# Kernel tuning notes

Measured on AMD Instinct MI355X. Metric: run time of the kernel, lower is better.

The kernel has to match this reference:

```python
import jax, jax.numpy as jnp
import numpy as np

B, N, M, H, D, DIM = 4, 2048, 512, 12, 64, 768
INNER = H * D
SCALE = D ** -0.5
NEG = -1e9
TEMP = 24.0


def setup_inputs() -> dict:
    key = jax.random.key(0)
    ks = jax.random.split(key, 8)
    x = jax.random.normal(ks[0], (B, N, DIM), jnp.float32)
    kx = jax.random.normal(ks[1], (B, M, DIM), jnp.float32)
    krd = jax.random.uniform(ks[2], (B, H, M, N), jnp.float32)
    clst = jax.random.normal(ks[3], (B, 1, DIM), jnp.float32)
    att_mask = jax.random.randint(ks[4], (B, H, N, M), 0, 2) > 0
    W_qkv = jax.random.normal(ks[5], (DIM, 3 * INNER), jnp.float32) / np.sqrt(DIM)
    W_out = jax.random.normal(ks[6], (INNER, DIM), jnp.float32) / np.sqrt(INNER)
    b_out = jnp.zeros((DIM,), jnp.float32)
    return {"x": x, "kx": kx, "krd": krd, "clst": clst, "att_mask": att_mask,
            "W_qkv": W_qkv, "W_out": W_out, "b_out": b_out}


def _qkv(t, W_qkv):
    # [b, n, dim] -> three [b, h, n, d]
    b, n, _ = t.shape
    qkv = (t @ W_qkv).reshape(b, n, 3, H, D)
    qkv = jnp.moveaxis(qkv, 2, 0)            # [3, b, n, h, d]
    qkv = jnp.transpose(qkv, (0, 1, 3, 2, 4))  # [3, b, h, n, d]
    return qkv[0], qkv[1], qkv[2]


def _merge(t):
    # [b, h, n, d] -> [b, n, h*d]
    b, h, n, d = t.shape
    return jnp.transpose(t, (0, 2, 1, 3)).reshape(b, n, h * d)


def reference(x, kx, krd, clst, att_mask, W_qkv, W_out, b_out):
    t_q, t_k, t_v = _qkv(x, W_qkv)
    k_q, k_k, k_v = _qkv(kx, W_qkv)
    c_q, _, _ = _qkv(clst, W_qkv)

    krd_T = jnp.transpose(krd, (0, 1, 3, 2))  # [b, h, N, M]

    # branch 1: instance queries vs kernel keys
    dots = jnp.einsum('bhid,bhjd->bhij', t_q, k_k) * SCALE
    dots = jnp.where(att_mask, NEG, dots)
    attn_hot = jax.nn.softmax(dots * TEMP, axis=-1) * krd_T
    attn = jax.nn.softmax(dots, axis=-1) * krd_T
    att_out = _merge(jnp.einsum('bhij,bhjd->bhid', attn, k_v))

    # branch 2: kernel queries vs instance keys
    k_dots = jnp.einsum('bhid,bhjd->bhij', k_q, t_k) * SCALE
    k_dots = jnp.where(jnp.transpose(att_mask, (0, 1, 3, 2)), NEG, k_dots)
    k_attn = jax.nn.softmax(k_dots, axis=-1) * krd
    k_out = _merge(jnp.einsum('bhij,bhjd->bhid', k_attn, t_v))

    # branch 3: cluster query vs kernel keys
    c_dots = jnp.einsum('bhid,bhjd->bhij', c_q, k_k) * SCALE
    c_dots = jnp.where(att_mask[:, :, :1], NEG, c_dots)
    c_attn = jax.nn.softmax(c_dots, axis=-1)
    c_out = _merge(jnp.einsum('bhij,bhjd->bhid', c_attn, k_v))

    proj = lambda t: t @ W_out + b_out
    return (proj(att_out), proj(k_out), proj(c_out),
            jnp.transpose(attn_hot, (0, 1, 3, 2)))
```

## Files before the change

kernel.cpp:

```cpp
#include <hip/hip_runtime.h>
#include <hip/hip_bf16.h>
#include <cmath>
#include <cstdint>

#define B_ 4
#define N_ 2048
#define M_ 512
#define H_ 12
#define D_ 64
#define DIM_ 768
#define QKV_ 2304
#define SCALE_ 0.125f
#define NEG_ -1e9f
#define TEMP_ 24.0f

typedef __attribute__((ext_vector_type(8))) short bf16x8;
typedef __attribute__((ext_vector_type(4))) float f32x4;

__device__ __forceinline__ short f2bf(float f) {
  union { float f; unsigned u; } v; v.f = f;
  unsigned r = v.u + 0x7fffu + ((v.u >> 16) & 1u);
  return (short)(r >> 16);
}
__device__ __forceinline__ float bf2f(short s) {
  union { unsigned u; float f; } v; v.u = ((unsigned)(unsigned short)s) << 16;
  return v.f;
}
#define MFMA16(a, b, c) __builtin_amdgcn_mfma_f32_16x16x32_bf16(a, b, c, 0, 0, 0)

__device__ __forceinline__ int xcd_swizzle(int orig, int nwg) {
  int qd = nwg >> 3, r = nwg & 7;
  int xcd = orig & 7, pos = orig >> 3;
  return (xcd < r ? xcd * (qd + 1) : r * (qd + 1) + (xcd - r) * qd) + pos;
}

__global__ __launch_bounds__(256) void wsplit_t(
    const float* __restrict__ W, int K, int Ncols,
    short* __restrict__ Wt_h, short* __restrict__ Wt_l) {
  __shared__ float t[32][33];
  const int n0 = blockIdx.x * 32, k0 = blockIdx.y * 32;
  const int tid = threadIdx.x;
  for (int e = tid; e < 1024; e += 256) {
    int r = e >> 5, c = e & 31;
    t[r][c] = W[(size_t)(k0 + r) * Ncols + n0 + c];
  }
  __syncthreads();
  for (int e = tid; e < 1024; e += 256) {
    int r = e >> 5, c = e & 31;
    float f = t[c][r];
    short hi = f2bf(f);
    short lo = f2bf(f - bf2f(hi));
    size_t o = (size_t)(n0 + r) * K + k0 + c;
    Wt_h[o] = hi; Wt_l[o] = lo;
  }
}

__global__ __launch_bounds__(256) void fsplit(
    const float* __restrict__ in, short* __restrict__ ho,
    short* __restrict__ lo_, int n4) {
  int stride = gridDim.x * 256;
  for (int i = blockIdx.x * 256 + threadIdx.x; i < n4; i += stride) {
    float4 f = ((const float4*)in)[i];
    short h0 = f2bf(f.x), h1 = f2bf(f.y), h2 = f2bf(f.z), h3 = f2bf(f.w);
    short l0 = f2bf(f.x - bf2f(h0)), l1 = f2bf(f.y - bf2f(h1));
    short l2 = f2bf(f.z - bf2f(h2)), l3 = f2bf(f.w - bf2f(h3));
    ((short4*)ho)[i] = make_short4(h0, h1, h2, h3);
    ((short4*)lo_)[i] = make_short4(l0, l1, l2, l3);
  }
}

__global__ __launch_bounds__(256) void mask_pack(
    const int* __restrict__ mask, unsigned* __restrict__ pm) {
  const size_t total = (size_t)B_ * H_ * N_ * M_;
  const size_t stride = (size_t)gridDim.x * blockDim.x;
  const int lane = threadIdx.x & 63;
  for (size_t i = (size_t)blockIdx.x * blockDim.x + threadIdx.x; i < total;
       i += stride) {
    unsigned long long bal = __ballot(mask[i] != 0);
    if (lane == 0) *(unsigned long long*)(pm + (i >> 5)) = bal;
  }
}

__global__ __launch_bounds__(256) void qkv_mfma(
    const short* __restrict__ Ahp, const short* __restrict__ Alp,
    const short* __restrict__ Wth, const short* __restrict__ Wtl,
    int rowsPerB, int totalRows,
    short* __restrict__ qh, short* __restrict__ ql,
    short* __restrict__ kh, short* __restrict__ kl,
    short* __restrict__ vt) {
  __shared__ __align__(16) short As_h[128 * 40], As_l[128 * 40];
  __shared__ __align__(16) short Bs_h[128 * 40], Bs_l[128 * 40];
  const int nwg = gridDim.x * gridDim.y;
  const int nb = xcd_swizzle(blockIdx.y * gridDim.x + blockIdx.x, nwg);
  const int gx = gridDim.x;
  const int r0 = (nb / gx) * 128, c0 = (nb % gx) * 128;
  const int tid = threadIdx.x;
  const int w = tid >> 6, ln = tid & 63, q = ln >> 4, l15 = ln & 15;
  const int wM = (w & 1) * 64, wN = (w >> 1) * 64;
  const f32x4 z = {0.f, 0.f, 0.f, 0.f};
  f32x4 acc[4][4];
  for (int i = 0; i < 4; i++)
    for (int j = 0; j < 4; j++) acc[i][j] = z;
  for (int k0 = 0; k0 < DIM_; k0 += 32) {
    for (int e = tid; e < 512; e += 256) {
      int row = e >> 2, c = e & 3;
      int ar = r0 + row; if (ar >= totalRows) ar = totalRows - 1;
      size_t ga = (size_t)ar * DIM_ + k0 + c * 8;
      size_t gb = (size_t)(c0 + row) * DIM_ + k0 + c * 8;
      int o = row * 40 + c * 8;
      *(uint4*)(As_h + o) = *(const uint4*)(Ahp + ga);
      *(uint4*)(As_l + o) = *(const uint4*)(Alp + ga);
      *(uint4*)(Bs_h + o) = *(const uint4*)(Wth + gb);
      *(uint4*)(Bs_l + o) = *(const uint4*)(Wtl + gb);
    }
    __syncthreads();
    bf16x8 ah[4], al[4], bhf[4], blf[4];
    for (int mt = 0; mt < 4; mt++) {
      int o = (wM + mt * 16 + l15) * 40 + q * 8;
      ah[mt] = *(const bf16x8*)(As_h + o);
      al[mt] = *(const bf16x8*)(As_l + o);
    }
    for (int nt = 0; nt < 4; nt++) {
      int o = (wN + nt * 16 + l15) * 40 + q * 8;
      bhf[nt] = *(const bf16x8*)(Bs_h + o);
      blf[nt] = *(const bf16x8*)(Bs_l + o);
    }
    for (int mt = 0; mt < 4; mt++)
      for (int nt = 0; nt < 4; nt++) {
        f32x4 c = acc[mt][nt];
        c = MFMA16(ah[mt], bhf[nt], c);
        c = MFMA16(ah[mt], blf[nt], c);
        c = MFMA16(al[mt], bhf[nt], c);
        acc[mt][nt] = c;
      }
    __syncthreads();
  }
  for (int mt = 0; mt < 4; mt++)
    for (int nt = 0; nt < 4; nt++)
      for (int r = 0; r < 4; r++) {
        int gr = r0 + wM + mt * 16 + q * 4 + r;
        if (gr >= totalRows) continue;
        int gc = c0 + wN + nt * 16 + l15;
        int which = gc / DIM_;
        int rem = gc - which * DIM_;
        int hh = rem >> 6, d = rem & 63;
        int b = gr / rowsPerB, n = gr - b * rowsPerB;
        float v = acc[mt][nt][r];
        short hi = f2bf(v);
        if (which == 2) {
          vt[(((size_t)b * H_ + hh) * 64 + d) * rowsPerB + n] = hi;
        } else {
          short lo = f2bf(v - bf2f(hi));
          size_t o = (((size_t)b * H_ + hh) * rowsPerB + n) * 64 + d;
          if (which == 0) { qh[o] = hi; ql[o] = lo; }
          else           { kh[o] = hi; kl[o] = lo; }
        }
      }
}

__global__ __launch_bounds__(256) void proj_mfma(
    const short* __restrict__ Ahp, const short* __restrict__ Alp,
    const short* __restrict__ Bth, const short* __restrict__ Btl,
    const float* __restrict__ bias, float* __restrict__ C, int totalRows) {
  __shared__ __align__(16) short As_h[128 * 40], As_l[128 * 40];
  __shared__ __align__(16) short Bs_h[128 * 40], Bs_l[128 * 40];
  const int nwg = gridDim.x * gridDim.y;
  const int nb = xcd_swizzle(blockIdx.y * gridDim.x + blockIdx.x, nwg);
  const int gx = gridDim.x;
  const int r0 = (nb / gx) * 128, c0 = (nb % gx) * 128;
  const int tid = threadIdx.x;
  const int w = tid >> 6, ln = tid & 63, q = ln >> 4, l15 = ln & 15;
  const int wM = (w & 1) * 64, wN = (w >> 1) * 64;
  const f32x4 z = {0.f, 0.f, 0.f, 0.f};
  f32x4 acc[4][4];
  for (int i = 0; i < 4; i++)
    for (int j = 0; j < 4; j++) acc[i][j] = z;
  for (int k0 = 0; k0 < DIM_; k0 += 32) {
    for (int e = tid; e < 512; e += 256) {
      int row = e >> 2, c = e & 3;
      int ar = r0 + row; if (ar >= totalRows) ar = totalRows - 1;
      size_t ga = (size_t)ar * DIM_ + k0 + c * 8;
      size_t gb = (size_t)(c0 + row) * DIM_ + k0 + c * 8;
      int o = row * 40 + c * 8;
      *(uint4*)(As_h + o) = *(const uint4*)(Ahp + ga);
      *(uint4*)(As_l + o) = *(const uint4*)(Alp + ga);
      *(uint4*)(Bs_h + o) = *(const uint4*)(Bth + gb);
      *(uint4*)(Bs_l + o) = *(const uint4*)(Btl + gb);
    }
    __syncthreads();
    bf16x8 ah[4], al[4], bhf[4], blf[4];
    for (int mt = 0; mt < 4; mt++) {
      int o = (wM + mt * 16 + l15) * 40 + q * 8;
      ah[mt] = *(const bf16x8*)(As_h + o);
      al[mt] = *(const bf16x8*)(As_l + o);
    }
    for (int nt = 0; nt < 4; nt++) {
      int o = (wN + nt * 16 + l15) * 40 + q * 8;
      bhf[nt] = *(const bf16x8*)(Bs_h + o);
      blf[nt] = *(const bf16x8*)(Bs_l + o);
    }
    for (int mt = 0; mt < 4; mt++)
      for (int nt = 0; nt < 4; nt++) {
        f32x4 c = acc[mt][nt];
        c = MFMA16(ah[mt], bhf[nt], c);
        c = MFMA16(ah[mt], blf[nt], c);
        c = MFMA16(al[mt], bhf[nt], c);
        acc[mt][nt] = c;
      }
    __syncthreads();
  }
  for (int mt = 0; mt < 4; mt++)
    for (int nt = 0; nt < 4; nt++)
      for (int r = 0; r < 4; r++) {
        int gr = r0 + wM + mt * 16 + q * 4 + r;
        if (gr >= totalRows) continue;
        int gc = c0 + wN + nt * 16 + l15;
        C[(size_t)gr * DIM_ + gc] = acc[mt][nt][r] + bias[gc];
      }
}

__global__ __launch_bounds__(512, 4) void branch1_mfma(
    const short* __restrict__ tqh, const short* __restrict__ tql,
    const short* __restrict__ kkh, const short* __restrict__ kkl,
    const short* __restrict__ kvt, const float* __restrict__ krd,
    const unsigned* __restrict__ pm, float* __restrict__ out3,
    short* __restrict__ amh, short* __restrict__ aml) {
  __shared__ __align__(16) float sc[32 * 520];
  __shared__ unsigned mskw[512];
  __shared__ float rowM[32], inv1[32], inv2[32];
  short* P2h = (short*)sc;
  short* P2l = P2h + 32 * 520;
  const int b = blockIdx.z, h = blockIdx.y, n0 = blockIdx.x * 32;
  const size_t bhi = (size_t)b * H_ + h;
  const int tid = threadIdx.x;
  const int w = tid >> 6, ln = tid & 63, q = ln >> 4, l15 = ln & 15;
  const float* krd0 = krd + bhi * M_ * N_;
  mskw[tid] = pm[(bhi * N_ + n0) * 16 + tid];
  {
    bf16x8 ah[2][2], al[2][2];
    for (int mt = 0; mt < 2; mt++) {
      const short* ap = tqh + ((bhi * N_ + n0 + mt * 16 + l15) * D_ + q * 8);
      const short* ap2 = tql + ((bhi * N_ + n0 + mt * 16 + l15) * D_ + q * 8);
      ah[mt][0] = *(const bf16x8*)(ap);
      ah[mt][1] = *(const bf16x8*)(ap + 32);
      al[mt][0] = *(const bf16x8*)(ap2);
      al[mt][1] = *(const bf16x8*)(ap2 + 32);
    }
    for (int t = 0; t < 4; t++) {
      int ct = w * 4 + t;
      const short* bp = kkh + ((bhi * M_ + ct * 16 + l15) * D_ + q * 8);
      const short* bp2 = kkl + ((bhi * M_ + ct * 16 + l15) * D_ + q * 8);
      bf16x8 bh0 = *(const bf16x8*)(bp);
      bf16x8 bh1 = *(const bf16x8*)(bp + 32);
      bf16x8 bl0 = *(const bf16x8*)(bp2);
      bf16x8 bl1 = *(const bf16x8*)(bp2 + 32);
      for (int mt = 0; mt < 2; mt++) {
        f32x4 a = {0.f, 0.f, 0.f, 0.f};
        a = MFMA16(ah[mt][0], bh0, a); a = MFMA16(ah[mt][1], bh1, a);
        a = MFMA16(ah[mt][0], bl0, a); a = MFMA16(ah[mt][1], bl1, a);
        a = MFMA16(al[mt][0], bh0, a); a = MFMA16(al[mt][1], bh1, a);
        for (int r = 0; r < 4; r++) {
          int row = mt * 16 + q * 4 + r;
          sc[row * 520 + ((ct * 16 + l15) ^ ((row >> 2) & 7))] = a[r];
        }
      }
    }
  }
  const int pi = tid & 31, pg = tid >> 5;
  float kr[32];
#pragma unroll
  for (int t = 0; t < 32; t++)
    kr[t] = __builtin_nontemporal_load(
        krd0 + (size_t)(pg * 32 + t) * N_ + n0 + pi);
  __syncthreads();
  {
    int i = tid >> 4, jl = tid & 15;
    int sw = (i >> 2) & 7;
    float* scr = sc + i * 520;
    const unsigned* mrow = mskw + i * 16;
    float mx = -INFINITY;
    for (int j = jl; j < M_; j += 16) {
      float dv = scr[j ^ sw];
      dv = ((mrow[j >> 5] >> (j & 31)) & 1) ? NEG_ : dv * SCALE_;
      scr[j ^ sw] = dv;
      mx = fmaxf(mx, dv);
    }
    for (int o = 8; o >= 1; o >>= 1) mx = fmaxf(mx, __shfl_xor(mx, o, 16));
    float s1 = 0.f, s2 = 0.f;
    for (int j = jl; j < M_; j += 16) {
      float e2 = __expf(scr[j ^ sw] - mx);
      scr[j ^ sw] = e2;
      float x2 = e2 * e2, x4 = x2 * x2, x8 = x4 * x4, x16 = x8 * x8;
      s1 += x16 * x8;
      s2 += e2;
    }
    for (int o = 8; o >= 1; o >>= 1) {
      s1 += __shfl_xor(s1, o, 16);
      s2 += __shfl_xor(s2, o, 16);
    }
    if (jl == 0) { inv1[i] = 1.f / s1; inv2[i] = 1.f / s2; }
  }
  __syncthreads();
  {
    float rv[32];
    int sw2 = (pi >> 2) & 7;
#pragma unroll
    for (int t = 0; t < 32; t++)
      rv[t] = sc[pi * 520 + ((pg * 32 + t) ^ sw2)];
    __syncthreads();
    float v1 = inv1[pi], v2 = inv2[pi];
    float* o3 = out3 + bhi * M_ * N_ + n0 + pi;
#pragma unroll
    for (int t = 0; t < 32; t += 2) {
      int j = pg * 32 + t;
      float e2a = rv[t], e2b = rv[t + 1];
      float a2 = e2a * e2a, a4 = a2 * a2, a8 = a4 * a4, a16 = a8 * a8;
      float b2 = e2b * e2b, b4 = b2 * b2, b8 = b4 * b4, b16 = b8 * b8;
      __builtin_nontemporal_store(a16 * a8 * v1 * kr[t], o3 + (size_t)j * N_);
      __builtin_nontemporal_store(b16 * b8 * v1 * kr[t + 1],
                                  o3 + (size_t)(j + 1) * N_);
      float p0 = e2a * v2 * kr[t];
      float p1 = e2b * v2 * kr[t + 1];
      short h0 = f2bf(p0), h1 = f2bf(p1);
      short lo0 = f2bf(p0 - bf2f(h0)), lo1 = f2bf(p1 - bf2f(h1));
      *(short2*)(P2h + pi * 520 + j) = make_short2(h0, h1);
      *(short2*)(P2l + pi * 520 + j) = make_short2(lo0, lo1);
    }
  }
  __syncthreads();
  {
    const int dc = w & 3, nh = w >> 2;
    f32x4 o0 = {0.f, 0.f, 0.f, 0.f}, o1 = {0.f, 0.f, 0.f, 0.f};
    const short* vbase = kvt + ((bhi * 64 + dc * 16 + l15) * (size_t)M_ + q * 8);
    const short* ph = P2h + (nh * 16 + l15) * 520 + q * 8;
    const short* pl = P2l + (nh * 16 + l15) * 520 + q * 8;
    for (int kc = 0; kc < 16; kc += 2) {
      bf16x8 pa0 = *(const bf16x8*)(ph + kc * 32);
      bf16x8 pl0 = *(const bf16x8*)(pl + kc * 32);
      bf16x8 bv0 = *(const bf16x8*)(vbase + kc * 32);
      o0 = MFMA16(pa0, bv0, o0);
      o0 = MFMA16(pl0, bv0, o0);
      bf16x8 pa1 = *(const bf16x8*)(ph + (kc + 1) * 32);
      bf16x8 pl1 = *(const bf16x8*)(pl + (kc + 1) * 32);
      bf16x8 bv1 = *(const bf16x8*)(vbase + (kc + 1) * 32);
      o1 = MFMA16(pa1, bv1, o1);
      o1 = MFMA16(pl1, bv1, o1);
    }
    o0 += o1;
    for (int r = 0; r < 4; r++) {
      float v = o0[r];
      short hi = f2bf(v), lo = f2bf(v - bf2f(hi));
      size_t o = ((size_t)b * N_ + n0 + nh * 16 + q * 4 + r) * DIM_ +
                 h * 64 + dc * 16 + l15;
      amh[o] = hi; aml[o] = lo;
    }
  }
}

__global__ __launch_bounds__(256) void branch2_mfma(
    const short* __restrict__ kqh, const short* __restrict__ kql,
    const short* __restrict__ tkh, const short* __restrict__ tkl,
    const short* __restrict__ tvt, const float* __restrict__ krd,
    const unsigned* __restrict__ pm, short* __restrict__ kmh,
    short* __restrict__ kml) {
  __shared__ __align__(16) float sc[32 * 136];
  __shared__ unsigned mskw[128];
  __shared__ float rowM[32], rowL[32], alph[32];
  short* P2h = (short*)sc;
  short* P2l = P2h + 32 * 136;
  const int b = blockIdx.z, h = blockIdx.y, m0 = blockIdx.x * 32;
  const size_t bhi = (size_t)b * H_ + h;
  const int tid = threadIdx.x;
  const int w = tid >> 6, ln = tid & 63, q = ln >> 4, l15 = ln & 15;
  const float* krd0 = krd + (bhi * M_ + m0) * N_;
  const int mword = m0 >> 5;
  bf16x8 Ah[2][2], Al[2][2];
  for (int mt = 0; mt < 2; mt++)
    for (int kc = 0; kc < 2; kc++) {
      size_t o = (bhi * M_ + m0 + mt * 16 + l15) * D_ + kc * 32 + q * 8;
      Ah[mt][kc] = *(const bf16x8*)(kqh + o);
      Al[mt][kc] = *(const bf16x8*)(kql + o);
    }
  if (tid < 32) { rowM[tid] = -INFINITY; rowL[tid] = 0.f; }
  const f32x4 z = {0.f, 0.f, 0.f, 0.f};
  f32x4 oa[2]; oa[0] = z; oa[1] = z;
  __syncthreads();
  for (int n0 = 0; n0 < N_; n0 += 128) {
    if (tid < 128) mskw[tid] = pm[(bhi * N_ + n0 + tid) * 16 + mword];
    for (int t = 0; t < 2; t++) {
      int ct = w * 2 + t;
      const short* bp = tkh + ((bhi * N_ + n0 + ct * 16 + l15) * D_ + q * 8);
      const short* bp2 = tkl + ((bhi * N_ + n0 + ct * 16 + l15) * D_ + q * 8);
      bf16x8 bh0 = *(const bf16x8*)(bp), bh1 = *(const bf16x8*)(bp + 32);
      bf16x8 bl0 = *(const bf16x8*)(bp2), bl1 = *(const bf16x8*)(bp2 + 32);
      for (int mt = 0; mt < 2; mt++) {
        f32x4 a = {0.f, 0.f, 0.f, 0.f};
        a = MFMA16(Ah[mt][0], bh0, a); a = MFMA16(Ah[mt][1], bh1, a);
        a = MFMA16(Ah[mt][0], bl0, a); a = MFMA16(Ah[mt][1], bl1, a);
        a = MFMA16(Al[mt][0], bh0, a); a = MFMA16(Al[mt][1], bh1, a);
        for (int r = 0; r < 4; r++)
          sc[(mt * 16 + q * 4 + r) * 136 + ct * 16 + l15] = a[r];
      }
    }
    __syncthreads();
    {
      int i = tid >> 3, jl = tid & 7;
      float mx = -INFINITY;
      for (int j = jl; j < 128; j += 8) {
        float s = sc[i * 136 + j];
        s = ((mskw[j] >> i) & 1) ? NEG_ : s * SCALE_;
        sc[i * 136 + j] = s;
        mx = fmaxf(mx, s);
      }
      for (int o = 4; o >= 1; o >>= 1) mx = fmaxf(mx, __shfl_xor(mx, o, 8));
      float mold = rowM[i];
      float mnew = fmaxf(mold, mx);
      float sum = 0.f;
      for (int j = jl; j < 128; j += 8) {
        float p = __expf(sc[i * 136 + j] - mnew);
        sc[i * 136 + j] = p;
        sum += p;
      }
      for (int o = 4; o >= 1; o >>= 1) sum += __shfl_xor(sum, o, 8);
      if (jl == 0) {
        float al = (mold == -INFINITY) ? 0.f : __expf(mold - mnew);
        alph[i] = al;
        rowL[i] = rowL[i] * al + sum;
        rowM[i] = mnew;
      }
    }
    __syncthreads();
    {
      float rv[16], kv2[16];
      const int j = tid & 127;
      const int ib = tid >> 7;
#pragma unroll
      for (int t = 0; t < 16; t++) {
        rv[t] = sc[(ib + 2 * t) * 136 + j];
        kv2[t] = __builtin_nontemporal_load(
            krd0 + (size_t)(ib + 2 * t) * N_ + n0 + j);
      }
      __syncthreads();
#pragma unroll
      for (int t = 0; t < 16; t++) {
        int i = ib + 2 * t;
        float p2 = rv[t] * kv2[t];
        short hi = f2bf(p2), lo = f2bf(p2 - bf2f(hi));
        P2h[i * 136 + j] = hi;
        P2l[i * 136 + j] = lo;
      }
    }
    __syncthreads();
    {
      for (int mt = 0; mt < 2; mt++) {
        f32x4 t = oa[mt];
        for (int r = 0; r < 4; r++) t[r] *= alph[mt * 16 + q * 4 + r];
        for (int kc = 0; kc < 4; kc++) {
          bf16x8 pa = *(const bf16x8*)(P2h + (mt * 16 + l15) * 136 + kc * 32 + q * 8);
          bf16x8 pl = *(const bf16x8*)(P2l + (mt * 16 + l15) * 136 + kc * 32 + q * 8);
          bf16x8 bv = *(const bf16x8*)(tvt + ((bhi * 64 + w * 16 + l15) * (size_t)N_ + n0 + kc * 32 + q * 8));
          t = MFMA16(pa, bv, t);
          t = MFMA16(pl, bv, t);
        }
        oa[mt] = t;
      }
    }
    __syncthreads();
  }
  for (int mt = 0; mt < 2; mt++)
    for (int r = 0; r < 4; r++) {
      int row = mt * 16 + q * 4 + r;
      float v = oa[mt][r] / rowL[row];
      short hi = f2bf(v), lo = f2bf(v - bf2f(hi));
      size_t o = ((size_t)b * M_ + m0 + row) * DIM_ + h * 64 + w * 16 + l15;
      kmh[o] = hi; kml[o] = lo;
    }
}

__global__ __launch_bounds__(256) void branch3_k(
    const short* __restrict__ cqh, const short* __restrict__ cql,
    const short* __restrict__ kkh, const short* __restrict__ kkl,
    const short* __restrict__ kvt, const unsigned* __restrict__ pm,
    short* __restrict__ cmh, short* __restrict__ cml) {
  const int h = blockIdx.x, b = blockIdx.y;
  __shared__ float qv[64];
  __shared__ float p[512];
  __shared__ float wr1[4], wr2[4];
  __shared__ float ored[4][64];
  const size_t bhi = (size_t)b * H_ + h;
  const int tid = threadIdx.x;
  if (tid < 64) qv[tid] = bf2f(cqh[bhi * 64 + tid]) + bf2f(cql[bhi * 64 + tid]);
  __syncthreads();
  const unsigned* m0p = pm + bhi * N_ * 16;
  for (int j = tid; j < 512; j += 256) {
    float acc = 0;
    for (int kk = 0; kk < 64; kk++)
      acc += qv[kk] * (bf2f(kkh[(bhi * M_ + j) * 64 + kk]) +
                       bf2f(kkl[(bhi * M_ + j) * 64 + kk]));
    acc *= SCALE_;
    if ((m0p[j >> 5] >> (j & 31)) & 1) acc = NEG_;
    p[j] = acc;
  }
  __syncthreads();
  float mx = fmaxf(p[tid], p[tid + 256]);
  for (int o = 32; o >= 1; o >>= 1) mx = fmaxf(mx, __shfl_xor(mx, o, 64));
  if ((tid & 63) == 0) wr1[tid >> 6] = mx;
  __syncthreads();
  mx = fmaxf(fmaxf(wr1[0], wr1[1]), fmaxf(wr1[2], wr1[3]));
  float e0 = __expf(p[tid] - mx), e1 = __expf(p[tid + 256] - mx);
  float s = e0 + e1;
  for (int o = 32; o >= 1; o >>= 1) s += __shfl_xor(s, o, 64);
  p[tid] = e0; p[tid + 256] = e1;
  if ((tid & 63) == 0) wr2[tid >> 6] = s;
  __syncthreads();
  float invS = 1.f / (wr2[0] + wr2[1] + wr2[2] + wr2[3]);
  int dd = tid & 63, gg = tid >> 6;
  float o = 0;
  for (int j = gg; j < 512; j += 4)
    o += p[j] * bf2f(kvt[(bhi * 64 + dd) * (size_t)M_ + j]);
  ored[gg][dd] = o;
  __syncthreads();
  if (gg == 0) {
    float r = (ored[0][dd] + ored[1][dd] + ored[2][dd] + ored[3][dd]) * invS;
    short hi = f2bf(r), lo = f2bf(r - bf2f(hi));
    cmh[(size_t)b * DIM_ + h * 64 + dd] = hi;
    cml[(size_t)b * DIM_ + h * 64 + dd] = lo;
  }
}

extern "C" void kernel_launch(void* const* d_in, const int* in_sizes, int n_in,
                              void* d_out, int out_size, void* d_ws,
                              size_t ws_size, hipStream_t stream) {
  const float* x = (const float*)d_in[0];
  const float* kx = (const float*)d_in[1];
  const float* krd = (const float*)d_in[2];
  const float* clst = (const float*)d_in[3];
  const int* mask = (const int*)d_in[4];
  const float* Wqkv = (const float*)d_in[5];
  const float* Wout = (const float*)d_in[6];
  const float* bout = (const float*)d_in[7];

  short* p = (short*)d_ws;
  auto alloc = [&](size_t n) { short* r = p; p += n; return r; };
  short* Wq_h = alloc(2304ull * 768); short* Wq_l = alloc(2304ull * 768);
  short* Wo_h = alloc(768ull * 768);  short* Wo_l = alloc(768ull * 768);
  short* tq_h = alloc(6291456); short* tq_l = alloc(6291456);
  short* tk_h = alloc(6291456); short* tk_l = alloc(6291456);
  short* tv_t = alloc(6291456);
  short* kq_h = alloc(1572864); short* kq_l = alloc(1572864);
  short* kk_h = alloc(1572864); short* kk_l = alloc(1572864);
  short* kv_t = alloc(1572864);
  short* cq_h = alloc(3072); short* cq_l = alloc(3072);
  short* ck_h = alloc(3072); short* ck_l = alloc(3072);
  short* cv_t = alloc(3072);
  short* am_h = alloc(6291456); short* am_l = alloc(6291456);
  short* km_h = alloc(1572864); short* km_l = alloc(1572864);
  short* cm_h = alloc(3072); short* cm_l = alloc(3072);

  float* out0 = (float*)d_out;
  float* out1 = out0 + 6291456;
  float* out2 = out1 + 1572864;
  float* out3 = out2 + 3072;

  wsplit_t<<<dim3(72, 24), 256, 0, stream>>>(Wqkv, DIM_, QKV_, Wq_h, Wq_l);
  wsplit_t<<<dim3(24, 24), 256, 0, stream>>>(Wout, DIM_, DIM_, Wo_h, Wo_l);

  short* xs_h = am_h, *xs_l = am_l;
  short* kxs_h = km_h, *kxs_l = km_l;
  short* cs_h = cm_h, *cs_l = cm_l;
  fsplit<<<dim3(2048), 256, 0, stream>>>(x, xs_h, xs_l, B_ * N_ * DIM_ / 4);
  fsplit<<<dim3(1536), 256, 0, stream>>>(kx, kxs_h, kxs_l, B_ * M_ * DIM_ / 4);
  fsplit<<<dim3(3), 256, 0, stream>>>(clst, cs_h, cs_l, B_ * DIM_ / 4);

  qkv_mfma<<<dim3(18, 64), 256, 0, stream>>>(xs_h, xs_l, Wq_h, Wq_l, N_,
                                             B_ * N_, tq_h, tq_l, tk_h, tk_l,
                                             tv_t);
  qkv_mfma<<<dim3(18, 16), 256, 0, stream>>>(kxs_h, kxs_l, Wq_h, Wq_l, M_,
                                             B_ * M_, kq_h, kq_l, kk_h, kk_l,
                                             kv_t);
  qkv_mfma<<<dim3(18, 1), 256, 0, stream>>>(cs_h, cs_l, Wq_h, Wq_l, 1, B_,
                                            cq_h, cq_l, ck_h, ck_l, cv_t);

  unsigned* pmask = (unsigned*)Wq_h;
  mask_pack<<<dim3(2048), 256, 0, stream>>>(mask, pmask);

  branch1_mfma<<<dim3(N_ / 32, H_, B_), 512, 0, stream>>>(
      tq_h, tq_l, kk_h, kk_l, kv_t, krd, pmask, out3, am_h, am_l);
  branch2_mfma<<<dim3(M_ / 32, H_, B_), 256, 0, stream>>>(
      kq_h, kq_l, tk_h, tk_l, tv_t, krd, pmask, km_h, km_l);
  branch3_k<<<dim3(H_, B_), 256, 0, stream>>>(cq_h, cq_l, kk_h, kk_l, kv_t,
                                              pmask, cm_h, cm_l);

  proj_mfma<<<dim3(6, 64), 256, 0, stream>>>(am_h, am_l, Wo_h, Wo_l, bout,
                                             out0, B_ * N_);
  proj_mfma<<<dim3(6, 16), 256, 0, stream>>>(km_h, km_l, Wo_h, Wo_l, bout,
                                             out1, B_ * M_);
  proj_mfma<<<dim3(6, 1), 256, 0, stream>>>(cm_h, cm_l, Wo_h, Wo_l, bout,
                                            out2, B_);
}
```

Before: 1.207 ms.

## Split branch2 attention over key dimension with separate combine kernel

Branch 2 previously ran one block per 32 kernel-query rows per head (768 blocks), each looping over all 2048 instance keys. The loop is now split four ways along the key dimension, giving four times as many blocks, each writing partial outputs plus row max and sum to scratch. A new combine kernel merges the partials with log-sum-exp weighting and writes the hi/lo bf16 outputs. This raises occupancy and parallelism on a long serial loop, at the cost of an extra launch and scratch traffic; the scratch reuses the out0/out1 buffers before the projection kernels overwrite them.

After: 1.168 ms. 1.03x faster.

```diff
diff --git a/kernel.cpp b/kernel.cpp
--- a/kernel.cpp
+++ b/kernel.cpp
@@ -13,6 +13,7 @@
 #define SCALE_ 0.125f
 #define NEG_ -1e9f
 #define TEMP_ 24.0f
+#define NSPLIT_ 4
 
 typedef __attribute__((ext_vector_type(8))) short bf16x8;
 typedef __attribute__((ext_vector_type(4))) float f32x4;
@@ -361,15 +362,18 @@
     const short* __restrict__ kqh, const short* __restrict__ kql,
     const short* __restrict__ tkh, const short* __restrict__ tkl,
     const short* __restrict__ tvt, const float* __restrict__ krd,
-    const unsigned* __restrict__ pm, short* __restrict__ kmh,
-    short* __restrict__ kml) {
+    const unsigned* __restrict__ pm, float* __restrict__ pO,
+    float* __restrict__ pML) {
   __shared__ __align__(16) float sc[32 * 136];
   __shared__ unsigned mskw[128];
   __shared__ float rowM[32], rowL[32], alph[32];
   short* P2h = (short*)sc;
   short* P2l = P2h + 32 * 136;
-  const int b = blockIdx.z, h = blockIdx.y, m0 = blockIdx.x * 32;
+  const int b = blockIdx.z, h = blockIdx.y;
+  const int mblk = blockIdx.x >> 2, split = blockIdx.x & 3;
+  const int m0 = mblk * 32;
   const size_t bhi = (size_t)b * H_ + h;
+  const int pidx = ((int)bhi * 16 + mblk) * NSPLIT_ + split;
   const int tid = threadIdx.x;
   const int w = tid >> 6, ln = tid & 63, q = ln >> 4, l15 = ln & 15;
   const float* krd0 = krd + (bhi * M_ + m0) * N_;
@@ -385,7 +389,8 @@
   const f32x4 z = {0.f, 0.f, 0.f, 0.f};
   f32x4 oa[2]; oa[0] = z; oa[1] = z;
   __syncthreads();
-  for (int n0 = 0; n0 < N_; n0 += 128) {
+  const int nbeg = split * (N_ / NSPLIT_), nend = nbeg + N_ / NSPLIT_;
+  for (int n0 = nbeg; n0 < nend; n0 += 128) {
     if (tid < 128) mskw[tid] = pm[(bhi * N_ + n0 + tid) * 16 + mword];
     for (int t = 0; t < 2; t++) {
       int ct = w * 2 + t;
@@ -467,14 +472,64 @@
     }
     __syncthreads();
   }
+  float* po = pO + (size_t)pidx * 2048;
   for (int mt = 0; mt < 2; mt++)
     for (int r = 0; r < 4; r++) {
       int row = mt * 16 + q * 4 + r;
-      float v = oa[mt][r] / rowL[row];
-      short hi = f2bf(v), lo = f2bf(v - bf2f(hi));
-      size_t o = ((size_t)b * M_ + m0 + row) * DIM_ + h * 64 + w * 16 + l15;
-      kmh[o] = hi; kml[o] = lo;
-    }
+      po[row * 64 + w * 16 + l15] = oa[mt][r];
+    }
+  if (tid < 32) {
+    pML[(size_t)pidx * 64 + tid] = rowM[tid];
+    pML[(size_t)pidx * 64 + 32 + tid] = rowL[tid];
+  }
+}
+
+__global__ __launch_bounds__(256) void b2_combine(
+    const float* __restrict__ pO, const float* __restrict__ pML,
+    short* __restrict__ kmh, short* __restrict__ kml) {
+  const int mblk = blockIdx.x, h = blockIdx.y, b = blockIdx.z;
+  const size_t bhi = (size_t)b * H_ + h;
+  const int base = ((int)bhi * 16 + mblk) * NSPLIT_;
+  __shared__ float mS[NSPLIT_][32], lS[NSPLIT_][32], wgt[NSPLIT_][32], invL[32];
+  const int tid = threadIdx.x;
+  if (tid < 32 * NSPLIT_) {
+    int s = tid >> 5, r = tid & 31;
+    mS[s][r] = pML[(size_t)(base + s) * 64 + r];
+    lS[s][r] = pML[(size_t)(base + s) * 64 + 32 + r];
+  }
+  __syncthreads();
+  if (tid < 32) {
+    float Mv = mS[0][tid];
+    for (int s = 1; s < NSPLIT_; s++) Mv = fmaxf(Mv, mS[s][tid]);
+    float L = 0.f;
+    for (int s = 0; s < NSPLIT_; s++) {
+      float wv = __expf(mS[s][tid] - Mv);
+      wgt[s][tid] = wv;
+      L += lS[s][tid] * wv;
+    }
+    invL[tid] = 1.f / L;
+  }
+  __syncthreads();
+  const int row = tid >> 3, c0 = (tid & 7) * 8;
+  float acc[8] = {0, 0, 0, 0, 0, 0, 0, 0};
+  for (int s = 0; s < NSPLIT_; s++) {
+    float wv = wgt[s][row];
+    const float* src = pO + (size_t)(base + s) * 2048 + row * 64 + c0;
+    float4 a = *(const float4*)(src);
+    float4 bq = *(const float4*)(src + 4);
+    acc[0] += a.x * wv;  acc[1] += a.y * wv;
+    acc[2] += a.z * wv;  acc[3] += a.w * wv;
+    acc[4] += bq.x * wv; acc[5] += bq.y * wv;
+    acc[6] += bq.z * wv; acc[7] += bq.w * wv;
+  }
+  float il = invL[row];
+  size_t o = ((size_t)b * M_ + mblk * 32 + row) * DIM_ + h * 64 + c0;
+#pragma unroll
+  for (int e = 0; e < 8; e++) {
+    float v = acc[e] * il;
+    short hi = f2bf(v), lo = f2bf(v - bf2f(hi));
+    kmh[o + e] = hi; kml[o + e] = lo;
+  }
 }
 
 __global__ __launch_bounds__(256) void branch3_k(
@@ -586,8 +641,13 @@
 
   branch1_mfma<<<dim3(N_ / 32, H_, B_), 512, 0, stream>>>(
       tq_h, tq_l, kk_h, kk_l, kv_t, krd, pmask, out3, am_h, am_l);
-  branch2_mfma<<<dim3(M_ / 32, H_, B_), 256, 0, stream>>>(
-      kq_h, kq_l, tk_h, tk_l, tv_t, krd, pmask, km_h, km_l);
+
+  float* pO = out0;
+  float* pML = out1;
+  branch2_mfma<<<dim3((M_ / 32) * NSPLIT_, H_, B_), 256, 0, stream>>>(
+      kq_h, kq_l, tk_h, tk_l, tv_t, krd, pmask, pO, pML);
+  b2_combine<<<dim3(M_ / 32, H_, B_), 256, 0, stream>>>(pO, pML, km_h, km_l);
+
   branch3_k<<<dim3(H_, B_), 256, 0, stream>>>(cq_h, cq_l, kk_h, kk_l, kv_t,
                                               pmask, cm_h, cm_l);
 
```
